# Kernel optimization log

Hardware: AMD Instinct MI355X
Metric: run time of the kernel (lower is better)

## Reference

```python
import jax, jax.numpy as jnp
import numpy as np

B, S, E, H = 4, 2048, 1024, 16
Dh = E // H
EPS = 1e-5


def setup_inputs() -> dict:
    key = jax.random.key(0)
    ks = jax.random.split(key, 16)
    w = lambda k, shp: jax.random.normal(k, shp, dtype=jnp.float32) * 0.02
    return {
        "x": jax.random.normal(ks[0], (B, S, E), dtype=jnp.float32),
        "Wq": w(ks[1], (E, E)), "bq": jnp.zeros((E,), jnp.float32),
        "Wk": w(ks[2], (E, E)), "bk": jnp.zeros((E,), jnp.float32),
        "Wv": w(ks[3], (E, E)), "bv": jnp.zeros((E,), jnp.float32),
        "Wo": w(ks[4], (E, E)), "bo": jnp.zeros((E,), jnp.float32),
        "an1_a": jnp.ones((1, S, 1), jnp.float32),
        "an1_b": jnp.zeros((1, S, 1), jnp.float32),
        "W1": w(ks[5], (2 * E, E)), "b1": jnp.zeros((2 * E,), jnp.float32),
        "W2": w(ks[6], (E, 2 * E)), "b2": jnp.zeros((E,), jnp.float32),
        "an2_a": jnp.ones((1, S, 1), jnp.float32),
        "an2_b": jnp.zeros((1, S, 1), jnp.float32),
    }


def adaptive_norm(x, a, b):
    # AdaptiveNorm((1, N_s, 1)): normalize over embedding dim, per-position affine.
    mu = jnp.mean(x, axis=-1, keepdims=True)
    var = jnp.mean(jnp.square(x - mu), axis=-1, keepdims=True)
    return a * (x - mu) * jax.lax.rsqrt(var + EPS) + b


def reference(x, Wq, bq, Wk, bk, Wv, bv, Wo, bo, an1_a, an1_b, W1, b1, W2, b2, an2_a, an2_b):
    scale = 1.0 / np.sqrt(E / H)
    # QKV projections -> (B, S, H, Dh)
    q = (x @ Wq.T + bq).reshape(B, S, H, Dh)
    k = (x @ Wk.T + bk).reshape(B, S, H, Dh)
    v = (x @ Wv.T + bv).reshape(B, S, H, Dh)
    # scaled dot-product attention (materializes B,H,S,S like the original)
    scores = jnp.einsum("bshd,bthd->bhst", q, k) * scale
    probs = jax.nn.softmax(scores, axis=-1)
    attn = jnp.einsum("bhst,bthd->bshd", probs, v).reshape(B, S, E)
    attn = attn @ Wo.T + bo
    # residual + adaptive norm (dropout is identity in eval mode)
    h = adaptive_norm(attn + x, an1_a, an1_b)
    ff = jax.nn.relu(h @ W1.T + b1) @ W2.T + b2
    out = adaptive_norm(ff + h, an2_a, an2_b)
    return out
```

## Files before the change

### kernel.cpp

```cpp
#include <hip/hip_runtime.h>


typedef __attribute__((ext_vector_type(8))) short s16x8;
typedef __attribute__((ext_vector_type(4))) short s16x4;
typedef __attribute__((ext_vector_type(4))) unsigned short u16x4;
typedef __attribute__((ext_vector_type(4))) float f32x4;

__device__ __forceinline__ float bf2f(unsigned short u) {
  unsigned int v = ((unsigned int)u) << 16;
  return __builtin_bit_cast(float, v);
}
__device__ __forceinline__ unsigned short f2bf(float f) {
  unsigned int u = __builtin_bit_cast(unsigned int, f);
  u += 0x7fffu + ((u >> 16) & 1u);
  return (unsigned short)(u >> 16);
}
__device__ __forceinline__ unsigned int pkbf_trunc(float f0, float f1) {
  return __builtin_amdgcn_perm(__builtin_bit_cast(unsigned int, f1),
                               __builtin_bit_cast(unsigned int, f0), 0x07060302u);
}
__device__ __forceinline__ f32x4 mfma16(s16x8 a, s16x8 b, f32x4 c) {
  return __builtin_amdgcn_mfma_f32_16x16x32_bf16(a, b, c, 0, 0, 0);
}
__device__ __forceinline__ void gl2lds16(const unsigned short* g, unsigned short* l) {
  __builtin_amdgcn_global_load_lds(
      (const __attribute__((address_space(1))) unsigned int*)(g),
      (__attribute__((address_space(3))) unsigned int*)(l), 16, 0, 0);
}

__global__ void detect_dtype(const unsigned int* __restrict__ x, int* __restrict__ flag) {
  const int tid = threadIdx.x;
  int cnt = 0;
  for (int i = tid; i < 2048; i += 256) {
    const unsigned e = (x[i] >> 7) & 0xFF;
    cnt += (e >= 100 && e <= 150) ? 1 : 0;
  }
#pragma unroll
  for (int off = 32; off >= 1; off >>= 1) cnt += __shfl_xor(cnt, off);
  __shared__ int red[4];
  if ((tid & 63) == 0) red[tid >> 6] = cnt;
  __syncthreads();
  if (tid == 0) *flag = ((red[0] + red[1] + red[2] + red[3]) > 1536) ? 1 : 0;
}

struct CvtArgs {
  const void* src[17];
  unsigned short* dst[17];
  int cum4[18];
};

__global__ __launch_bounds__(256) void cvt_all(CvtArgs a, const int* __restrict__ flag, int total4) {
  const int i = blockIdx.x * 256 + threadIdx.x;
  if (i >= total4) return;
  int lo = 0, hi = 17;
  while (hi - lo > 1) {
    const int mid = (lo + hi) >> 1;
    if (i >= a.cum4[mid]) lo = mid; else hi = mid;
  }
  const int off4 = i - a.cum4[lo];
  if (*flag) {
    const u16x4* s = (const u16x4*)a.src[lo];
    *(u16x4*)&a.dst[lo][off4 * 4] = s[off4];
  } else {
    const float4* s = (const float4*)a.src[lo];
    const float4 v = s[off4];
    u16x4 o;
    o[0] = f2bf(v.x); o[1] = f2bf(v.y); o[2] = f2bf(v.z); o[3] = f2bf(v.w);
    *(u16x4*)&a.dst[lo][off4 * 4] = o;
  }
}

#define QOFF 8388608L
#define SCALE2 0.18033688011f

template <int EPI>
__device__ __forceinline__ void gemm_epi_elem(
    unsigned short* __restrict__ out, const unsigned short* __restrict__ resid,
    int N, long gmb, int gn, const f32x4& a, float bv) {
  if constexpr (EPI == 2) {
#pragma unroll
    for (int r = 0; r < 4; ++r) {
      const long gm = gmb + r;
      out[gm * N + gn] = f2bf(a[r] + bv + bf2f(resid[gm * N + gn]));
    }
  } else if constexpr (EPI == 3) {
#pragma unroll
    for (int r = 0; r < 4; ++r)
      out[(gmb + r) * N + gn] = f2bf(fmaxf(a[r] + bv, 0.0f));
  } else {
    const int seg = gn >> 10;
    const int nn = gn & 1023;
    if (seg == 0) {
#pragma unroll
      for (int r = 0; r < 4; ++r)
        out[(gmb + r) * 1024 + nn] = f2bf((a[r] + bv) * SCALE2);
    } else if (seg == 1) {
#pragma unroll
      for (int r = 0; r < 4; ++r)
        (out + QOFF)[(gmb + r) * 1024 + nn] = f2bf(a[r] + bv);
    } else {
      const int h = nn >> 6, d = nn & 63;
      const long b = gmb >> 11;
      const int s = (int)(gmb & 2047);
      s16x4 pv;
#pragma unroll
      for (int r = 0; r < 4; ++r) pv[r] = (short)f2bf(a[r] + bv);
      *(s16x4*)&(out + 2 * QOFF)[((b * 16 + h) * 64L + d) * 2048 + s] = pv;
    }
  }
}

template <int EPI>
__global__ __launch_bounds__(512, 1) void gemm256(
    const unsigned short* __restrict__ A, const unsigned short* __restrict__ W,
    const unsigned short* __restrict__ bias, const unsigned short* __restrict__ resid,
    unsigned short* __restrict__ out, int M, int N, int K) {
  extern __shared__ unsigned short sh[];
  const int tid = threadIdx.x;
  const int lane = tid & 63;
  const int wave = tid >> 6;
  const int qd = lane >> 4;
  const int c = lane & 15;
  const int wm = (wave >> 2) * 64;
  const int wn = (wave & 3) * 32;

  const int nx = gridDim.x, ny = gridDim.y;
  const int nwg = nx * ny;
  int lin = blockIdx.y * nx + blockIdx.x;
  lin = (lin & 7) * (nwg >> 3) + (lin >> 3);
  const int by = lin % ny;
  const int bx = lin / ny;
  const long m0 = (long)by * 256;
  const long n0 = (long)bx * 256;

  const int srow = tid >> 3;
  const int scc = ((tid & 7) ^ (srow & 7)) * 8;
  const unsigned short* Asrc = A + (m0 + srow) * (long)K + scc;
  const unsigned short* Wsrc = W + (n0 + srow) * (long)K + scc;
  const int lofs = tid * 8;

  f32x4 acc[8][4] = {};
  const int NT = K >> 6;

  auto stage = [&](int tt, int r) {
    unsigned short* dst = sh + (tt & 1) * 32768;
    const long kof = (long)tt * 64;
    if (r < 2)      gl2lds16(Asrc + (long)r * 64 * K + kof, dst + r * 4096 + lofs);
    else if (r < 6) gl2lds16(Wsrc + (long)(r - 2) * 64 * K + kof,
                             dst + 16384 + (r - 2) * 4096 + lofs);
    else            gl2lds16(Asrc + (long)(r - 4) * 64 * K + kof, dst + (r - 4) * 4096 + lofs);
  };

#pragma unroll
  for (int r = 0; r < 8; ++r) stage(0, r);

  for (int t = 0; t < NT; ++t) {
    const unsigned short* Ab = sh + (t & 1) * 32768;
    const unsigned short* Bb = Ab + 16384;
    const bool dost = (t + 1 < NT);
    s16x8 af[4][2], bf0[2][2], bf1[2][2];

    asm volatile("s_waitcnt vmcnt(4)\n\ts_barrier" ::: "memory");
#pragma unroll
    for (int mt = 0; mt < 4; ++mt)
#pragma unroll
      for (int ks = 0; ks < 2; ++ks)
        af[mt][ks] = *(const s16x8*)&Ab[(wm + mt * 16 + c) * 64 +
                                        (((ks * 4 + qd) ^ (c & 7)) * 8)];
#pragma unroll
    for (int nt = 0; nt < 2; ++nt)
#pragma unroll
      for (int ks = 0; ks < 2; ++ks)
        bf0[nt][ks] = *(const s16x8*)&Bb[(wn + nt * 16 + c) * 64 +
                                         (((ks * 4 + qd) ^ (c & 7)) * 8)];
    if (dost) { stage(t + 1, 0); stage(t + 1, 1); }
    __builtin_amdgcn_s_setprio(1);
#pragma unroll
    for (int mt = 0; mt < 4; ++mt)
#pragma unroll
      for (int nt = 0; nt < 2; ++nt)
#pragma unroll
        for (int ks = 0; ks < 2; ++ks)
          acc[mt][nt] = mfma16(af[mt][ks], bf0[nt][ks], acc[mt][nt]);
    __builtin_amdgcn_s_setprio(0);

    if (dost) asm volatile("s_waitcnt vmcnt(4)\n\ts_barrier" ::: "memory");
    else      asm volatile("s_waitcnt vmcnt(2)\n\ts_barrier" ::: "memory");
#pragma unroll
    for (int nt = 0; nt < 2; ++nt)
#pragma unroll
      for (int ks = 0; ks < 2; ++ks)
        bf1[nt][ks] = *(const s16x8*)&Bb[(128 + wn + nt * 16 + c) * 64 +
                                         (((ks * 4 + qd) ^ (c & 7)) * 8)];
    if (dost) { stage(t + 1, 2); stage(t + 1, 3); }
    __builtin_amdgcn_s_setprio(1);
#pragma unroll
    for (int mt = 0; mt < 4; ++mt)
#pragma unroll
      for (int nt = 0; nt < 2; ++nt)
#pragma unroll
        for (int ks = 0; ks < 2; ++ks)
          acc[mt][2 + nt] = mfma16(af[mt][ks], bf1[nt][ks], acc[mt][2 + nt]);
    __builtin_amdgcn_s_setprio(0);

    if (dost) asm volatile("s_waitcnt vmcnt(4)\n\ts_barrier" ::: "memory");
    else      asm volatile("s_waitcnt vmcnt(0)\n\ts_barrier" ::: "memory");
#pragma unroll
    for (int mt = 0; mt < 4; ++mt)
#pragma unroll
      for (int ks = 0; ks < 2; ++ks)
        af[mt][ks] = *(const s16x8*)&Ab[(128 + wm + mt * 16 + c) * 64 +
                                        (((ks * 4 + qd) ^ (c & 7)) * 8)];
    if (dost) { stage(t + 1, 4); stage(t + 1, 5); }
    __builtin_amdgcn_s_setprio(1);
#pragma unroll
    for (int mt = 0; mt < 4; ++mt)
#pragma unroll
      for (int nt = 0; nt < 2; ++nt)
#pragma unroll
        for (int ks = 0; ks < 2; ++ks)
          acc[4 + mt][2 + nt] = mfma16(af[mt][ks], bf1[nt][ks], acc[4 + mt][2 + nt]);
    __builtin_amdgcn_s_setprio(0);

    asm volatile("s_barrier" ::: "memory");
    if (dost) { stage(t + 1, 6); stage(t + 1, 7); }
    __builtin_amdgcn_s_setprio(1);
#pragma unroll
    for (int mt = 0; mt < 4; ++mt)
#pragma unroll
      for (int nt = 0; nt < 2; ++nt)
#pragma unroll
        for (int ks = 0; ks < 2; ++ks)
          acc[4 + mt][nt] = mfma16(af[mt][ks], bf0[nt][ks], acc[4 + mt][nt]);
    __builtin_amdgcn_s_setprio(0);
  }

#pragma unroll
  for (int j = 0; j < 4; ++j) {
    const int gn = (int)n0 + (j >> 1) * 128 + wn + (j & 1) * 16 + c;
    const float bv = bf2f(bias[gn]);
#pragma unroll
    for (int i = 0; i < 8; ++i) {
      const long gmb = m0 + (i >> 2) * 128 + wm + (i & 3) * 16 + qd * 4;
      gemm_epi_elem<EPI>(out, resid, N, gmb, gn, acc[i][j], bv);
    }
  }
}

template <int EPI, int BM>
__global__ __launch_bounds__(512, 1) void gemm2(
    const unsigned short* __restrict__ A, const unsigned short* __restrict__ W,
    const unsigned short* __restrict__ bias, const unsigned short* __restrict__ resid,
    unsigned short* __restrict__ out, int M, int N, int K) {
  constexpr int BUFE = (BM + 256) * 64;
  extern __shared__ unsigned short sh[];

  const int tid = threadIdx.x;
  const int lane = tid & 63;
  const int wave = tid >> 6;
  const int qd = lane >> 4;
  const int c = lane & 15;
  const int wr = (wave >> 2) * (BM / 2);
  const int wc = (wave & 3) * 64;

  const int nx = gridDim.x, ny = gridDim.y;
  const int nwg = nx * ny;
  int lin = blockIdx.y * nx + blockIdx.x;
  lin = (lin & 7) * (nwg >> 3) + (lin >> 3);
  const int by = lin % ny;
  const int bx = lin / ny;
  const long m0 = (long)by * BM;
  const long n0 = (long)bx * 256;

  const int srow = tid >> 3;
  const int scc = ((tid & 7) ^ (srow & 7)) * 8;
  const unsigned short* Asrc = A + (m0 + srow) * (long)K + scc;
  const unsigned short* Wsrc = W + (n0 + srow) * (long)K + scc;
  const int lofs = tid * 8;

  f32x4 acc[BM / 32][4] = {};
  const int NT = K >> 6;

  auto stA = [&](int sel, int tt, int q) {
    gl2lds16(Asrc + (long)q * 64 * K + (long)tt * 64, sh + sel * BUFE + q * 4096 + lofs);
  };
  auto stB = [&](int sel, int tt, int q) {
    gl2lds16(Wsrc + (long)q * 64 * K + (long)tt * 64,
             sh + sel * BUFE + BM * 64 + q * 4096 + lofs);
  };

  stB(0, 0, 0); stB(0, 0, 1); stB(0, 0, 2); stB(0, 0, 3); stA(0, 0, 0); stA(0, 0, 1);
  stB(1, 1, 0); stB(1, 1, 1); stB(1, 1, 2); stB(1, 1, 3); stA(1, 1, 0); stA(1, 1, 1);

  int cur = 0;
  for (int t = 0; t < NT; ++t) {
    const unsigned short* Ab = sh + cur * BUFE;
    const unsigned short* Bb = Ab + BM * 64;

    if (t + 1 < NT) asm volatile("s_waitcnt vmcnt(6)\n\ts_barrier" ::: "memory");
    else            asm volatile("s_waitcnt vmcnt(0)\n\ts_barrier" ::: "memory");
    s16x8 bfr[4][2], af[4][2];
#pragma unroll
    for (int nt = 0; nt < 4; ++nt)
#pragma unroll
      for (int ks = 0; ks < 2; ++ks)
        bfr[nt][ks] = *(const s16x8*)&Bb[(wc + nt * 16 + c) * 64 +
                                         (((ks * 4 + qd) ^ (c & 7)) * 8)];
#pragma unroll
    for (int mt = 0; mt < 4; ++mt)
#pragma unroll
      for (int ks = 0; ks < 2; ++ks)
        af[mt][ks] = *(const s16x8*)&Ab[(wr + mt * 16 + c) * 64 +
                                        (((ks * 4 + qd) ^ (c & 7)) * 8)];
    if (t + 2 < NT) {
      const int ns = (cur >= 1) ? cur - 1 : 2;
      stB(ns, t + 2, 0); stB(ns, t + 2, 1); stB(ns, t + 2, 2); stB(ns, t + 2, 3);
      stA(ns, t + 2, 0); stA(ns, t + 2, 1);
    }
    __builtin_amdgcn_s_setprio(1);
#pragma unroll
    for (int mt = 0; mt < 4; ++mt)
#pragma unroll
      for (int nt = 0; nt < 4; ++nt)
#pragma unroll
        for (int ks = 0; ks < 2; ++ks)
          acc[mt][nt] = mfma16(af[mt][ks], bfr[nt][ks], acc[mt][nt]);
    __builtin_amdgcn_s_setprio(0);
    cur = (cur + 1 == 3) ? 0 : cur + 1;
  }

#pragma unroll
  for (int nt = 0; nt < 4; ++nt) {
    const int gn = (int)n0 + wc + nt * 16 + c;
    const float bv = bf2f(bias[gn]);
#pragma unroll
    for (int mt = 0; mt < BM / 32; ++mt) {
      const long gmb = m0 + wr + mt * 16 + qd * 4;
      gemm_epi_elem<EPI>(out, resid, N, gmb, gn, acc[mt][nt], bv);
    }
  }
}

#define ATT_S 2048

__global__ __launch_bounds__(256)
__attribute__((amdgpu_waves_per_eu(2, 2))) void attn_fwd(
    const unsigned short* __restrict__ Q, const unsigned short* __restrict__ K,
    const unsigned short* __restrict__ VT, unsigned short* __restrict__ O) {
  __shared__ unsigned short SH[32768];
  unsigned short* Kb0 = SH;
  unsigned short* Kb1 = SH + 4096;
  unsigned short* Vb0 = SH + 8192;
  unsigned short* Vb1 = SH + 12288;
  unsigned short* Pl  = SH + 16384;

  const int bh = blockIdx.y;
  const int q0 = blockIdx.x * 256;
  const long b = bh >> 4;
  const int h = bh & 15;
  const unsigned short* Qg = Q + (b * 2048) * 1024 + h * 64;
  const unsigned short* Kg = K + (b * 2048) * 1024 + h * 64;
  const unsigned short* Vg = VT + (long)bh * 64 * 2048;

  const int tid = threadIdx.x;
  const int wave = tid >> 6, lane = tid & 63;
  const int qd = lane >> 4, c = lane & 15;
  const int mb = wave * 32;

  const int srow = tid >> 3;
  const int sccs = ((tid & 7) ^ (srow & 7)) * 8;

  s16x8 qf[2][2][2];
#pragma unroll
  for (int h2 = 0; h2 < 2; ++h2)
#pragma unroll
    for (int mt = 0; mt < 2; ++mt)
#pragma unroll
      for (int ks = 0; ks < 2; ++ks)
        qf[h2][mt][ks] = *(const s16x8*)&Qg[(long)(q0 + h2 * 128 + mb + mt * 16 + c) * 1024 +
                                            ks * 32 + qd * 8];

  s16x8 ones;
#pragma unroll
  for (int i = 0; i < 8; ++i) ones[i] = (short)0x3F80;

  f32x4 oacc[2][4][2] = {};
  f32x4 lacc[2][2] = {};

  gl2lds16(Kg + (long)srow * 1024 + sccs, &Kb0[tid * 8]);
  gl2lds16(Kg + (long)(srow + 32) * 1024 + sccs, &Kb0[(256 + tid) * 8]);
  gl2lds16(Vg + (long)srow * 2048 + sccs, &Vb0[tid * 8]);
  gl2lds16(Vg + (long)(srow + 32) * 2048 + sccs, &Vb0[(256 + tid) * 8]);

  for (int it = 0; it < 32; ++it) {
    const int p = it & 1;
    unsigned short* Kc = p ? Kb1 : Kb0;
    unsigned short* Vc = p ? Vb1 : Vb0;
    unsigned short* Kn = p ? Kb0 : Kb1;
    unsigned short* Vn = p ? Vb0 : Vb1;
    const int kvn = (it < 31) ? (it + 1) * 64 : 31 * 64;
    gl2lds16(Kg + (long)(kvn + srow) * 1024 + sccs, &Kn[tid * 8]);
    gl2lds16(Kg + (long)(kvn + srow + 32) * 1024 + sccs, &Kn[(256 + tid) * 8]);
    gl2lds16(Vg + (long)srow * 2048 + kvn + sccs, &Vn[tid * 8]);
    gl2lds16(Vg + (long)(srow + 32) * 2048 + kvn + sccs, &Vn[(256 + tid) * 8]);

    asm volatile("s_waitcnt vmcnt(4)\n\ts_barrier" ::: "memory");

    f32x4 sacc[2][4][2] = {};
#pragma unroll
    for (int ks = 0; ks < 2; ++ks) {
      const int ch = ((ks * 4 + qd) ^ (c & 7)) * 8;
      s16x8 kf[4];
#pragma unroll
      for (int tt = 0; tt < 4; ++tt)
        kf[tt] = *(const s16x8*)&Kc[(tt * 16 + c) * 64 + ch];
#pragma unroll
      for (int h2 = 0; h2 < 2; ++h2)
#pragma unroll
        for (int mt = 0; mt < 2; ++mt)
#pragma unroll
          for (int tt = 0; tt < 4; ++tt)
            sacc[h2][tt][mt] = mfma16(kf[tt], qf[h2][mt][ks], sacc[h2][tt][mt]);
    }

#pragma unroll
    for (int h2 = 0; h2 < 2; ++h2) {
      unsigned short* Ph = Pl + h2 * 8192;
#pragma unroll
      for (int mt = 0; mt < 2; ++mt) {
        const int ml = mb + mt * 16 + c;
#pragma unroll
        for (int tt = 0; tt < 4; ++tt) {
          unsigned int pk[2];
          pk[0] = pkbf_trunc(__builtin_amdgcn_exp2f(sacc[h2][tt][mt][0]),
                             __builtin_amdgcn_exp2f(sacc[h2][tt][mt][1]));
          pk[1] = pkbf_trunc(__builtin_amdgcn_exp2f(sacc[h2][tt][mt][2]),
                             __builtin_amdgcn_exp2f(sacc[h2][tt][mt][3]));
          const int chw = ((tt * 2 + (qd >> 1)) ^ (ml & 7)) * 8 + (qd & 1) * 4;
          *(uint2*)&Ph[ml * 64 + chw] = *(uint2*)pk;
        }
      }
    }
    asm volatile("s_waitcnt lgkmcnt(0)" ::: "memory");

#pragma unroll
    for (int ks = 0; ks < 2; ++ks) {
      const int vch = ((ks * 4 + qd) ^ (c & 7)) * 8;
      s16x8 vf[4];
#pragma unroll
      for (int dt = 0; dt < 4; ++dt)
        vf[dt] = *(const s16x8*)&Vc[(dt * 16 + c) * 64 + vch];
#pragma unroll
      for (int h2 = 0; h2 < 2; ++h2) {
        const unsigned short* Ph = Pl + h2 * 8192;
        s16x8 pf[2];
#pragma unroll
        for (int mt = 0; mt < 2; ++mt) {
          const int pr = mb + mt * 16 + c;
          pf[mt] = *(const s16x8*)&Ph[pr * 64 + (((ks * 4 + qd) ^ (pr & 7)) * 8)];
        }
#pragma unroll
        for (int mt = 0; mt < 2; ++mt) {
#pragma unroll
          for (int dt = 0; dt < 4; ++dt)
            oacc[h2][dt][mt] = mfma16(vf[dt], pf[mt], oacc[h2][dt][mt]);
          lacc[h2][mt] = mfma16(ones, pf[mt], lacc[h2][mt]);
        }
      }
    }

    asm volatile("s_barrier" ::: "memory");
  }

#pragma unroll
  for (int h2 = 0; h2 < 2; ++h2)
#pragma unroll
    for (int mt = 0; mt < 2; ++mt) {
      const float inv = 1.0f / lacc[h2][mt][0];
      const int s = q0 + h2 * 128 + mb + mt * 16 + c;
      const long ob = (b * (long)ATT_S + s) * 1024L + h * 64;
#pragma unroll
      for (int dt = 0; dt < 4; ++dt) {
        s16x4 ov;
#pragma unroll
        for (int r = 0; r < 4; ++r) ov[r] = (short)f2bf(oacc[h2][dt][mt][r] * inv);
        *(s16x4*)&O[ob + dt * 16 + qd * 4] = ov;
      }
    }
}

template <bool FINAL>
__global__ __launch_bounds__(256) void norm_affine(
    const unsigned short* __restrict__ X, const unsigned short* __restrict__ av,
    const unsigned short* __restrict__ bv, void* __restrict__ outv,
    const int* __restrict__ flag) {
  const int row = blockIdx.x;
  const int s = row & 2047;
  const unsigned short* xr = X + (long)row * 1024;
  const int tid = threadIdx.x;
  const u16x4 u = *(const u16x4*)&xr[tid * 4];
  float v[4];
  float s1 = 0.f, s2 = 0.f;
#pragma unroll
  for (int i = 0; i < 4; ++i) {
    v[i] = bf2f(u[i]);
    s1 += v[i];
    s2 += v[i] * v[i];
  }
#pragma unroll
  for (int off = 32; off >= 1; off >>= 1) {
    s1 += __shfl_xor(s1, off);
    s2 += __shfl_xor(s2, off);
  }
  __shared__ float red[8];
  const int wave = tid >> 6, lane = tid & 63;
  if (lane == 0) {
    red[wave * 2] = s1;
    red[wave * 2 + 1] = s2;
  }
  __syncthreads();
  s1 = red[0] + red[2] + red[4] + red[6];
  s2 = red[1] + red[3] + red[5] + red[7];
  const float mean = s1 * (1.0f / 1024.0f);
  const float var = fmaxf(s2 * (1.0f / 1024.0f) - mean * mean, 0.0f);
  const float rstd = rsqrtf(var + 1e-5f);
  const float aa = bf2f(av[s]), bb = bf2f(bv[s]);
  float o[4];
#pragma unroll
  for (int i = 0; i < 4; ++i) o[i] = aa * (v[i] - mean) * rstd + bb;
  bool as_bf16 = true;
  if constexpr (FINAL) as_bf16 = (*flag != 0);
  if (as_bf16) {
    u16x4 ob;
#pragma unroll
    for (int i = 0; i < 4; ++i) ob[i] = f2bf(o[i]);
    *(u16x4*)&((unsigned short*)outv)[(long)row * 1024 + tid * 4] = ob;
  } else {
    float4 of = {o[0], o[1], o[2], o[3]};
    *(float4*)&((float*)outv)[(long)row * 1024 + tid * 4] = of;
  }
}

extern "C" void kernel_launch(void* const* d_in, const int* in_sizes, int n_in,
                              void* d_out, int out_size, void* d_ws, size_t ws_size,
                              hipStream_t stream) {
  char* ws = (char*)d_ws;
  const size_t SZ = 8192ull * 1024 * 2;
  const size_t WSZ = 1024ull * 1024 * 2;

  unsigned short* xb   = (unsigned short*)(ws);
  unsigned short* qb   = (unsigned short*)(ws + SZ);
  unsigned short* kb   = (unsigned short*)(ws + 2 * SZ);
  unsigned short* vtb  = (unsigned short*)(ws + 3 * SZ);
  unsigned short* attn = (unsigned short*)(ws + 4 * SZ);
  unsigned short* hb   = (unsigned short*)(ws + 5 * SZ);
  unsigned short* r1   = qb;
  unsigned short* ffb  = kb;
  unsigned short* r2   = attn;

  char* wreg = ws + 6 * SZ;
  unsigned short* wqb = (unsigned short*)(wreg);
  unsigned short* w1b = (unsigned short*)(wreg + 4 * WSZ);
  unsigned short* w2b = (unsigned short*)(wreg + 6 * WSZ);
  unsigned short* wob = (unsigned short*)(wreg + 3 * WSZ);
  unsigned short* smal = (unsigned short*)(wreg + 8 * WSZ);
  unsigned short* bqb = smal;
  unsigned short* bkb = smal + 1024;
  unsigned short* bvb = smal + 2048;
  unsigned short* bob = smal + 3072;
  unsigned short* b1b = smal + 4096;
  unsigned short* b2b = smal + 6144;
  unsigned short* a1b = smal + 7168;
  unsigned short* g1b = smal + 9216;
  unsigned short* a2b = smal + 11264;
  unsigned short* g2b = smal + 13312;
  int* flag = (int*)(wreg + 8 * WSZ + 64 * 1024);

  CvtArgs ca;
  unsigned short* wkb = wqb + 1024 * 1024;
  unsigned short* wvb = wqb + 2 * 1024 * 1024;
  unsigned short* dsts[17] = {xb, wqb, bqb, wkb, bkb, wvb, bvb, wob, bob,
                              a1b, g1b, w1b, b1b, w2b, b2b, a2b, g2b};
  ca.cum4[0] = 0;
  for (int i = 0; i < 17; ++i) {
    ca.src[i] = d_in[i];
    ca.dst[i] = dsts[i];
    ca.cum4[i + 1] = ca.cum4[i] + in_sizes[i] / 4;
  }
  const int total4 = ca.cum4[17];

  static bool attr_set = false;
  if (!attr_set) {
    attr_set = true;
    hipFuncSetAttribute(reinterpret_cast<const void*>(gemm256<4>),
                        hipFuncAttributeMaxDynamicSharedMemorySize, 131072);
    hipFuncSetAttribute(reinterpret_cast<const void*>(gemm256<3>),
                        hipFuncAttributeMaxDynamicSharedMemorySize, 131072);
    hipFuncSetAttribute(reinterpret_cast<const void*>(gemm2<2, 128>),
                        hipFuncAttributeMaxDynamicSharedMemorySize, 147456);
  }

  dim3 blk(256);
  dim3 blk512(512);
  detect_dtype<<<1, blk, 0, stream>>>((const unsigned int*)d_in[0], flag);
  cvt_all<<<(total4 + 255) / 256, blk, 0, stream>>>(ca, flag, total4);

  gemm256<4><<<dim3(12, 32), blk512, 131072, stream>>>(xb, wqb, bqb, nullptr, qb, 8192, 3072, 1024);
  attn_fwd<<<dim3(8, 64), blk, 0, stream>>>(qb, kb, vtb, attn);
  gemm2<2, 128><<<dim3(4, 64), blk512, 147456, stream>>>(attn, wob, bob, xb, r1, 8192, 1024, 1024);
  norm_affine<false><<<8192, blk, 0, stream>>>(r1, a1b, g1b, hb, nullptr);
  gemm256<3><<<dim3(8, 32), blk512, 131072, stream>>>(hb, w1b, b1b, nullptr, ffb, 8192, 2048, 1024);
  gemm2<2, 128><<<dim3(4, 64), blk512, 147456, stream>>>(ffb, w2b, b2b, hb, r2, 8192, 1024, 2048);
  norm_affine<true><<<8192, blk, 0, stream>>>(r2, a2b, g2b, d_out, flag);
}
```

Measured before the change: 408.2 us.

## Restructure 256x256 GEMM into 8-phase ping-pong schedule with quadrant wave mapping

```diff
diff --git a/kernel.cpp b/kernel.cpp
--- a/kernel.cpp
+++ b/kernel.cpp
@@ -110,8 +110,12 @@
   }
 }
 
+#define GBAR asm volatile("s_barrier" ::: "memory")
+#define GLGKM0 do { asm volatile("s_waitcnt lgkmcnt(0)" ::: "memory"); \
+                    __builtin_amdgcn_sched_barrier(0); } while (0)
+
 template <int EPI>
-__global__ __launch_bounds__(512, 1) void gemm256(
+__global__ __launch_bounds__(512, 1) void gemm8ph(
     const unsigned short* __restrict__ A, const unsigned short* __restrict__ W,
     const unsigned short* __restrict__ bias, const unsigned short* __restrict__ resid,
     unsigned short* __restrict__ out, int M, int N, int K) {
@@ -121,8 +125,8 @@
   const int wave = tid >> 6;
   const int qd = lane >> 4;
   const int c = lane & 15;
-  const int wm = (wave >> 2) * 64;
-  const int wn = (wave & 3) * 32;
+  const int wvm = wave >> 2;
+  const int wvn = wave & 3;
 
   const int nx = gridDim.x, ny = gridDim.y;
   const int nwg = nx * ny;
@@ -137,43 +141,49 @@
   const int scc = ((tid & 7) ^ (srow & 7)) * 8;
   const unsigned short* Asrc = A + (m0 + srow) * (long)K + scc;
   const unsigned short* Wsrc = W + (n0 + srow) * (long)K + scc;
-  const int lofs = tid * 8;
 
   f32x4 acc[8][4] = {};
   const int NT = K >> 6;
-
-  auto stage = [&](int tt, int r) {
-    unsigned short* dst = sh + (tt & 1) * 32768;
-    const long kof = (long)tt * 64;
-    if (r < 2)      gl2lds16(Asrc + (long)r * 64 * K + kof, dst + r * 4096 + lofs);
-    else if (r < 6) gl2lds16(Wsrc + (long)(r - 2) * 64 * K + kof,
-                             dst + 16384 + (r - 2) * 4096 + lofs);
-    else            gl2lds16(Asrc + (long)(r - 4) * 64 * K + kof, dst + (r - 4) * 4096 + lofs);
+  const int NI = K >> 7;
+
+  auto stageHalf = [&](int t, int which) {
+    unsigned short* buf = sh + (t & 1) * 32768;
+    const long kof = (long)t * 64;
+    if (which < 2) {
+      unsigned short* d = buf + which * 8192;
+      const unsigned short* s = Asrc + (long)(which * 128) * K + kof;
+      gl2lds16(s, d + tid * 8);
+      gl2lds16(s + (long)64 * K, d + 4096 + tid * 8);
+    } else {
+      const int h = which - 2;
+      unsigned short* d = buf + 16384 + h * 8192;
+      const unsigned short* s = Wsrc + (long)(h * 128) * K + kof;
+      gl2lds16(s, d + tid * 8);
+      gl2lds16(s + (long)64 * K, d + 4096 + tid * 8);
+    }
   };
 
-#pragma unroll
-  for (int r = 0; r < 8; ++r) stage(0, r);
-
-  for (int t = 0; t < NT; ++t) {
-    const unsigned short* Ab = sh + (t & 1) * 32768;
-    const unsigned short* Bb = Ab + 16384;
-    const bool dost = (t + 1 < NT);
-    s16x8 af[4][2], bf0[2][2], bf1[2][2];
-
-    asm volatile("s_waitcnt vmcnt(4)\n\ts_barrier" ::: "memory");
+  auto rdA = [&](s16x8 (&af)[4][2], const unsigned short* Abase, int qm) {
 #pragma unroll
     for (int mt = 0; mt < 4; ++mt)
 #pragma unroll
-      for (int ks = 0; ks < 2; ++ks)
-        af[mt][ks] = *(const s16x8*)&Ab[(wm + mt * 16 + c) * 64 +
-                                        (((ks * 4 + qd) ^ (c & 7)) * 8)];
+      for (int ks = 0; ks < 2; ++ks) {
+        const int lr = qm * 64 + mt * 16 + c;
+        af[mt][ks] = *(const s16x8*)&Abase[wvm * 8192 + lr * 64 +
+                                           (((ks * 4 + qd) ^ (c & 7)) * 8)];
+      }
+  };
+  auto rdB = [&](s16x8 (&bf)[2][2], const unsigned short* Bbase, int qn) {
 #pragma unroll
     for (int nt = 0; nt < 2; ++nt)
 #pragma unroll
-      for (int ks = 0; ks < 2; ++ks)
-        bf0[nt][ks] = *(const s16x8*)&Bb[(wn + nt * 16 + c) * 64 +
-                                         (((ks * 4 + qd) ^ (c & 7)) * 8)];
-    if (dost) { stage(t + 1, 0); stage(t + 1, 1); }
+      for (int ks = 0; ks < 2; ++ks) {
+        const int lb = (wvn & 1) * 64 + qn * 32 + nt * 16 + c;
+        bf[nt][ks] = *(const s16x8*)&Bbase[(wvn >> 1) * 8192 + lb * 64 +
+                                           (((ks * 4 + qd) ^ (c & 7)) * 8)];
+      }
+  };
+  auto mfmaQ = [&](s16x8 (&af)[4][2], s16x8 (&bf)[2][2], int qm, int qn) {
     __builtin_amdgcn_s_setprio(1);
 #pragma unroll
     for (int mt = 0; mt < 4; ++mt)
@@ -181,68 +191,86 @@
       for (int nt = 0; nt < 2; ++nt)
 #pragma unroll
         for (int ks = 0; ks < 2; ++ks)
-          acc[mt][nt] = mfma16(af[mt][ks], bf0[nt][ks], acc[mt][nt]);
+          acc[qm * 4 + mt][qn * 2 + nt] =
+              mfma16(af[mt][ks], bf[nt][ks], acc[qm * 4 + mt][qn * 2 + nt]);
     __builtin_amdgcn_s_setprio(0);
-
-    if (dost) asm volatile("s_waitcnt vmcnt(4)\n\ts_barrier" ::: "memory");
-    else      asm volatile("s_waitcnt vmcnt(2)\n\ts_barrier" ::: "memory");
-#pragma unroll
-    for (int nt = 0; nt < 2; ++nt)
-#pragma unroll
-      for (int ks = 0; ks < 2; ++ks)
-        bf1[nt][ks] = *(const s16x8*)&Bb[(128 + wn + nt * 16 + c) * 64 +
-                                         (((ks * 4 + qd) ^ (c & 7)) * 8)];
-    if (dost) { stage(t + 1, 2); stage(t + 1, 3); }
-    __builtin_amdgcn_s_setprio(1);
-#pragma unroll
-    for (int mt = 0; mt < 4; ++mt)
-#pragma unroll
-      for (int nt = 0; nt < 2; ++nt)
-#pragma unroll
-        for (int ks = 0; ks < 2; ++ks)
-          acc[mt][2 + nt] = mfma16(af[mt][ks], bf1[nt][ks], acc[mt][2 + nt]);
-    __builtin_amdgcn_s_setprio(0);
-
-    if (dost) asm volatile("s_waitcnt vmcnt(4)\n\ts_barrier" ::: "memory");
-    else      asm volatile("s_waitcnt vmcnt(0)\n\ts_barrier" ::: "memory");
-#pragma unroll
-    for (int mt = 0; mt < 4; ++mt)
-#pragma unroll
-      for (int ks = 0; ks < 2; ++ks)
-        af[mt][ks] = *(const s16x8*)&Ab[(128 + wm + mt * 16 + c) * 64 +
-                                        (((ks * 4 + qd) ^ (c & 7)) * 8)];
-    if (dost) { stage(t + 1, 4); stage(t + 1, 5); }
-    __builtin_amdgcn_s_setprio(1);
-#pragma unroll
-    for (int mt = 0; mt < 4; ++mt)
-#pragma unroll
-      for (int nt = 0; nt < 2; ++nt)
-#pragma unroll
-        for (int ks = 0; ks < 2; ++ks)
-          acc[4 + mt][2 + nt] = mfma16(af[mt][ks], bf1[nt][ks], acc[4 + mt][2 + nt]);
-    __builtin_amdgcn_s_setprio(0);
-
-    asm volatile("s_barrier" ::: "memory");
-    if (dost) { stage(t + 1, 6); stage(t + 1, 7); }
-    __builtin_amdgcn_s_setprio(1);
-#pragma unroll
-    for (int mt = 0; mt < 4; ++mt)
-#pragma unroll
-      for (int nt = 0; nt < 2; ++nt)
-#pragma unroll
-        for (int ks = 0; ks < 2; ++ks)
-          acc[4 + mt][nt] = mfma16(af[mt][ks], bf0[nt][ks], acc[4 + mt][nt]);
-    __builtin_amdgcn_s_setprio(0);
-  }
-
-#pragma unroll
-  for (int j = 0; j < 4; ++j) {
-    const int gn = (int)n0 + (j >> 1) * 128 + wn + (j & 1) * 16 + c;
+  };
+
+  stageHalf(0, 0); stageHalf(0, 1); stageHalf(0, 2); stageHalf(0, 3);
+  stageHalf(1, 2); stageHalf(1, 3);
+  asm volatile("s_waitcnt vmcnt(4)" ::: "memory");
+  GBAR;
+
+  for (int i = 0; i < NI; ++i) {
+    const int t0 = 2 * i, t1 = 2 * i + 1;
+    const unsigned short* Ab0 = sh;
+    const unsigned short* Bb0 = sh + 16384;
+    const unsigned short* Ab1 = sh + 32768;
+    const unsigned short* Bb1 = sh + 32768 + 16384;
+    const bool last = (i == NI - 1);
+
+    s16x8 af[4][2], bfa[2][2], bfb[2][2];
+
+    rdA(af, Ab0, 0);
+    rdB(bfa, Bb0, 0);
+    stageHalf(t1, 0);
+    GBAR; GLGKM0;
+    mfmaQ(af, bfa, 0, 0);
+    GBAR;
+
+    rdB(bfb, Bb0, 1);
+    stageHalf(t1, 1);
+    GBAR; GLGKM0;
+    mfmaQ(af, bfb, 0, 1);
+    GBAR;
+
+    rdA(af, Ab0, 1);
+    if (!last) stageHalf(t0 + 2, 2);
+    GBAR; GLGKM0;
+    mfmaQ(af, bfb, 1, 1);
+    GBAR;
+
+    if (!last) stageHalf(t0 + 2, 3);
+    mfmaQ(af, bfa, 1, 0);
+    if (last) asm volatile("s_waitcnt vmcnt(0)" ::: "memory");
+    else      asm volatile("s_waitcnt vmcnt(4)" ::: "memory");
+    GBAR;
+
+    rdA(af, Ab1, 0);
+    rdB(bfa, Bb1, 0);
+    if (!last) stageHalf(t0 + 2, 0);
+    GBAR; GLGKM0;
+    mfmaQ(af, bfa, 0, 0);
+    GBAR;
+
+    rdB(bfb, Bb1, 1);
+    if (!last) stageHalf(t0 + 2, 1);
+    GBAR; GLGKM0;
+    mfmaQ(af, bfb, 0, 1);
+    GBAR;
+
+    rdA(af, Ab1, 1);
+    if (!last) stageHalf(t0 + 3, 2);
+    GBAR; GLGKM0;
+    mfmaQ(af, bfb, 1, 1);
+    GBAR;
+
+    if (!last) stageHalf(t0 + 3, 3);
+    mfmaQ(af, bfa, 1, 0);
+    if (last) asm volatile("s_waitcnt vmcnt(0)" ::: "memory");
+    else      asm volatile("s_waitcnt vmcnt(4)" ::: "memory");
+    GBAR;
+  }
+
+#pragma unroll
+  for (int in = 0; in < 4; ++in) {
+    const int gn = (int)n0 + (wvn >> 1) * 128 + (wvn & 1) * 64 + (in >> 1) * 32 +
+                   (in & 1) * 16 + c;
     const float bv = bf2f(bias[gn]);
 #pragma unroll
-    for (int i = 0; i < 8; ++i) {
-      const long gmb = m0 + (i >> 2) * 128 + wm + (i & 3) * 16 + qd * 4;
-      gemm_epi_elem<EPI>(out, resid, N, gmb, gn, acc[i][j], bv);
+    for (int im = 0; im < 8; ++im) {
+      const long gmb = m0 + wvm * 128 + (im >> 2) * 64 + (im & 3) * 16 + qd * 4;
+      gemm_epi_elem<EPI>(out, resid, N, gmb, gn, acc[im][in], bv);
     }
   }
 }
@@ -592,9 +620,9 @@
   static bool attr_set = false;
   if (!attr_set) {
     attr_set = true;
-    hipFuncSetAttribute(reinterpret_cast<const void*>(gemm256<4>),
+    hipFuncSetAttribute(reinterpret_cast<const void*>(gemm8ph<4>),
                         hipFuncAttributeMaxDynamicSharedMemorySize, 131072);
-    hipFuncSetAttribute(reinterpret_cast<const void*>(gemm256<3>),
+    hipFuncSetAttribute(reinterpret_cast<const void*>(gemm8ph<3>),
                         hipFuncAttributeMaxDynamicSharedMemorySize, 131072);
     hipFuncSetAttribute(reinterpret_cast<const void*>(gemm2<2, 128>),
                         hipFuncAttributeMaxDynamicSharedMemorySize, 147456);
@@ -605,11 +633,11 @@
   detect_dtype<<<1, blk, 0, stream>>>((const unsigned int*)d_in[0], flag);
   cvt_all<<<(total4 + 255) / 256, blk, 0, stream>>>(ca, flag, total4);
 
-  gemm256<4><<<dim3(12, 32), blk512, 131072, stream>>>(xb, wqb, bqb, nullptr, qb, 8192, 3072, 1024);
+  gemm8ph<4><<<dim3(12, 32), blk512, 131072, stream>>>(xb, wqb, bqb, nullptr, qb, 8192, 3072, 1024);
   attn_fwd<<<dim3(8, 64), blk, 0, stream>>>(qb, kb, vtb, attn);
   gemm2<2, 128><<<dim3(4, 64), blk512, 147456, stream>>>(attn, wob, bob, xb, r1, 8192, 1024, 1024);
   norm_affine<false><<<8192, blk, 0, stream>>>(r1, a1b, g1b, hb, nullptr);
-  gemm256<3><<<dim3(8, 32), blk512, 131072, stream>>>(hb, w1b, b1b, nullptr, ffb, 8192, 2048, 1024);
+  gemm8ph<3><<<dim3(8, 32), blk512, 131072, stream>>>(hb, w1b, b1b, nullptr, ffb, 8192, 2048, 1024);
   gemm2<2, 128><<<dim3(4, 64), blk512, 147456, stream>>>(ffb, w2b, b2b, hb, r2, 8192, 1024, 2048);
   norm_affine<true><<<8192, blk, 0, stream>>>(r2, a2b, g2b, d_out, flag);
 }
```

New measurement: 428.1 us. +4.9%, slower.
